# Optimization experiments

Measured on AMD Instinct MI355X. Metric: run time of the kernel, lower is better.

## Reference

```python
import jax, jax.numpy as jnp
import numpy as np
from jax import lax

B = 16384
NWIRES = 4


def _conv(x, w, b):
    # NCHW conv, stride 1, SAME padding (pad 1 for k=3)
    y = lax.conv_general_dilated(x, w, (1, 1), ((1, 1), (1, 1)),
                                 dimension_numbers=("NCHW", "OIHW", "NCHW"))
    return y + b[None, :, None, None]


def _pool2(x):
    b, c, h, w = x.shape
    return x.reshape(b, c, h // 2, 2, w // 2, 2).max(axis=(3, 5))


def _apply_1q(state, U, wire):
    # state: (B,2,2,2,2) complex; U: (B,2,2) complex
    s = jnp.moveaxis(state, wire + 1, -1)
    s = jnp.einsum("bij,b...j->b...i", U, s)
    return jnp.moveaxis(s, -1, wire + 1)


def _apply_cnot(state, c, t):
    s0 = jnp.take(state, 0, axis=c + 1)
    s1 = jnp.take(state, 1, axis=c + 1)
    ta = t + 1 if t < c else t  # target axis index after removing control axis
    s1 = jnp.flip(s1, axis=ta)
    return jnp.stack([s0, s1], axis=c + 1)


def _ry(th):
    c = jnp.cos(th / 2)
    s = jnp.sin(th / 2)
    U = jnp.stack([jnp.stack([c, -s], -1), jnp.stack([s, c], -1)], -2)
    return U.astype(jnp.complex64)


def _rz(th):
    e = jnp.exp(-0.5j * th.astype(jnp.complex64))
    z = jnp.zeros_like(e)
    return jnp.stack([jnp.stack([e, z], -1), jnp.stack([z, jnp.conj(e)], -1)], -2)


def _rx(th):
    c = jnp.cos(th / 2).astype(jnp.complex64)
    s = jnp.sin(th / 2).astype(jnp.complex64)
    return jnp.stack([jnp.stack([c, -1j * s], -1), jnp.stack([-1j * s, c], -1)], -2)


def _circuit(params):
    # params: (B, 16) -> PauliZ expvals (B, 4)
    b = params.shape[0]
    state = jnp.zeros((b, 16), jnp.complex64).at[:, 0].set(1.0).reshape(b, 2, 2, 2, 2)
    for i in range(NWIRES):
        state = _apply_1q(state, _ry(params[:, 4 * i + 0]), i)
        state = _apply_1q(state, _rz(params[:, 4 * i + 1]), i)
        state = _apply_1q(state, _rx(params[:, 4 * i + 2]), i)
        state = _apply_cnot(state, i, (i + 1) % NWIRES)
    probs = state.real ** 2 + state.imag ** 2  # (B,2,2,2,2)
    zs = []
    for i in range(NWIRES):
        p = probs.sum(axis=tuple(a for a in range(1, 5) if a != i + 1))  # (B,2)
        zs.append(p[:, 0] - p[:, 1])
    return jnp.stack(zs, axis=-1)


def setup_inputs() -> dict:
    key = jax.random.key(0)
    ks = jax.random.split(key, 12)
    d = {}
    d["x"] = jax.random.normal(ks[0], (B, 1, 28, 28), jnp.float32)
    d["conv1_w"] = jax.random.normal(ks[1], (4, 1, 3, 3), jnp.float32) * 0.3
    d["conv1_b"] = jax.random.normal(ks[2], (4,), jnp.float32) * 0.1
    d["conv2_w"] = jax.random.normal(ks[3], (4, 4, 3, 3), jnp.float32) * 0.15
    d["conv2_b"] = jax.random.normal(ks[4], (4,), jnp.float32) * 0.1
    d["pl_w"] = jax.random.normal(ks[5], (16, 196), jnp.float32) * 0.07
    d["pl_b"] = jax.random.normal(ks[6], (16,), jnp.float32) * 0.05
    d["ro_w"] = jax.random.normal(ks[7], (4, 4), jnp.float32) * 0.5
    d["ro_b"] = jax.random.normal(ks[8], (4,), jnp.float32) * 0.1
    d["bn_w"] = jnp.ones((4,), jnp.float32)
    d["bn_b"] = jnp.zeros((4,), jnp.float32)
    return d


def reference(x, conv1_w, conv1_b, conv2_w, conv2_b, pl_w, pl_b, ro_w, ro_b, bn_w, bn_b):
    h = _pool2(jax.nn.relu(_conv(x, conv1_w, conv1_b)))   # (B,4,14,14)
    h = _pool2(jax.nn.relu(_conv(h, conv2_w, conv2_b)))   # (B,4,7,7)
    flat = h.reshape(x.shape[0], -1)                      # (B,196)
    params = flat @ pl_w.T + pl_b                         # (B,16)
    z = _circuit(params)                                  # (B,4)
    out = z @ ro_w.T + ro_b                               # (B,4)
    mean = out.mean(0)
    var = out.var(0)  # biased, matches torch BN training normalization
    return (out - mean) / jnp.sqrt(var + 1e-5) * bn_w + bn_b
```

## Files before the change

### kernel.cpp

```cpp
#include <hip/hip_runtime.h>
#include <math.h>

#define BATCH 16384

typedef float v2f __attribute__((ext_vector_type(2)));

__device__ __forceinline__ v2f pk_fma(v2f a, v2f b, v2f c) {
  return __builtin_elementwise_fma(a, b, c);
}
__device__ __forceinline__ v2f pk_max(v2f a, v2f b) {
  return __builtin_elementwise_max(a, b);
}

__device__ __forceinline__ unsigned bf2(float lo, float hi) {
  unsigned a = __float_as_uint(lo);
  unsigned b = __float_as_uint(hi);
  a = (a + 0x7fffu + ((a >> 16) & 1u)) >> 16;
  b = (b + 0x7fffu + ((b >> 16) & 1u)) & 0xffff0000u;
  return a | b;
}

__global__ __launch_bounds__(256) void qnat_fused(
    const float* __restrict__ x,
    const float* __restrict__ w1,
    const float* __restrict__ b1,
    const float* __restrict__ w2,
    const float* __restrict__ b2,
    const float* __restrict__ plw,
    const float* __restrict__ plb,
    const float* __restrict__ rw,
    const float* __restrict__ rb,
    float* __restrict__ pre,
    float* __restrict__ stats)
{
  __shared__ __align__(16) float h1p[4][4 * 288 + 16];
  __shared__ __align__(16) float h2[4][4][200];
  __shared__ __align__(16) uint4 plw_tb[25 * 16];
  __shared__ float s_red[4][8];

  const int tid = threadIdx.x;
  const int w = tid >> 6;
  const int lane = tid & 63;
  const int base = (blockIdx.x * 4 + w) * 4;

  #pragma unroll
  for (int j = 0; j < 2; j++) {
    int s = tid + 256 * j;
    if (s < 400) {
      int tp = s >> 4;
      int k = s & 15;
      const float4* pr = (const float4*)(plw + k * 196);
      float4 a = pr[2 * tp];
      float4 b = (tp < 24) ? pr[2 * tp + 1] : make_float4(0.f, 0.f, 0.f, 0.f);
      plw_tb[s] = make_uint4(bf2(a.x, a.y), bf2(a.z, a.w),
                             bf2(b.x, b.y), bf2(b.z, b.w));
    }
  }

  {
    float4 z4 = make_float4(0.f, 0.f, 0.f, 0.f);
    float4* hz = (float4*)&h1p[w][0];
    #pragma unroll
    for (int t = 0; t < 5; t++) {
      int p = t * 64 + lane;
      if (p < 292) hz[p] = z4;
    }
    if (lane < 16) h2[w][lane >> 2][196 + (lane & 3)] = 0.0f;
  }
  __syncthreads();

  const int i = lane >> 2;
  const int q = lane & 3;
  const bool c1act = lane < 56;

  float4 pfa[4], pfb[4];
  float pe0[4], pe1[4];
  #pragma unroll
  for (int r = 0; r < 4; r++) {
    pfa[r] = make_float4(0,0,0,0); pfb[r] = make_float4(0,0,0,0);
    pe0[r] = 0.0f; pe1[r] = 0.0f;
  }

  if (c1act) {
    const float* xb = x + (size_t)base * 784;
    #pragma unroll
    for (int r = 0; r < 4; r++) {
      int row = 2 * i - 1 + r;
      if (0 <= row && row < 28) {
        const float* rp = xb + row * 28;
        pfa[r] = *(const float4*)(rp + 8 * q);
        if (q > 0) pe0[r] = rp[8 * q - 1];
        if (q < 3) {
          pfb[r] = *(const float4*)(rp + 8 * q + 4);
          pe1[r] = rp[8 * q + 8];
        }
      }
    }
  }

  for (int it = 0; it < 4; ++it) {
    if (c1act) {
      float win[4][10];
      #pragma unroll
      for (int r = 0; r < 4; r++) {
        win[r][0] = pe0[r];
        win[r][1] = pfa[r].x; win[r][2] = pfa[r].y;
        win[r][3] = pfa[r].z; win[r][4] = pfa[r].w;
        win[r][5] = pfb[r].x; win[r][6] = pfb[r].y;
        win[r][7] = pfb[r].z; win[r][8] = pfb[r].w;
        win[r][9] = pe1[r];
      }
      if (it != 3) {
        const float* xn = x + (size_t)(base + it + 1) * 784;
        #pragma unroll
        for (int r = 0; r < 4; r++) {
          int row = 2 * i - 1 + r;
          pfa[r] = make_float4(0,0,0,0);
          pfb[r] = make_float4(0,0,0,0);
          pe0[r] = 0.0f; pe1[r] = 0.0f;
          if (0 <= row && row < 28) {
            const float* rp = xn + row * 28;
            pfa[r] = *(const float4*)(rp + 8 * q);
            if (q > 0) pe0[r] = rp[8 * q - 1];
            if (q < 3) {
              pfb[r] = *(const float4*)(rp + 8 * q + 4);
              pe1[r] = rp[8 * q + 8];
            }
          }
        }
      }
      v2f P[4][9];
      #pragma unroll
      for (int r = 0; r < 4; r++)
        #pragma unroll
        for (int k = 0; k < 9; k++) P[r][k] = (v2f){win[r][k], win[r][k + 1]};

      float* hb = &h1p[w][18 * (i + 1) + 1 + 4 * q];
      #pragma unroll
      for (int c = 0; c < 4; c++) {
        const float* wc = w1 + c * 9;
        const v2f bias2 = (v2f){b1[c], b1[c]};
        v2f a0[4], a1[4];
        #pragma unroll
        for (int jj = 0; jj < 4; jj++) { a0[jj] = bias2; a1[jj] = bias2; }
        #pragma unroll
        for (int dy = 0; dy < 3; dy++)
          #pragma unroll
          for (int dx = 0; dx < 3; dx++) {
            const float wv = wc[dy * 3 + dx];
            const v2f wvv = (v2f){wv, wv};
            #pragma unroll
            for (int jj = 0; jj < 4; jj++) {
              a0[jj] = pk_fma(P[dy][2 * jj + dx],     wvv, a0[jj]);
              a1[jj] = pk_fma(P[dy + 1][2 * jj + dx], wvv, a1[jj]);
            }
          }
        float m[4];
        #pragma unroll
        for (int jj = 0; jj < 4; jj++) {
          v2f mm = pk_max(a0[jj], a1[jj]);
          m[jj] = fmaxf(fmaxf(mm.x, mm.y), 0.0f);
        }
        float* p = hb + 288 * c;
        if (q < 3) {
          p[0] = m[0];
          *(float2*)(p + 1) = make_float2(m[1], m[2]);
          p[3] = m[3];
        } else {
          p[0] = m[0];
          p[1] = m[1];
        }
      }
    }

    {
      const int jq = lane & 7;
      const int i2 = lane >> 3;
      if (i2 < 7 && jq < 7) {
        v2f acc[4][2];
        #pragma unroll
        for (int co = 0; co < 4; co++) {
          const v2f bb = (v2f){b2[co], b2[co]};
          acc[co][0] = bb; acc[co][1] = bb;
        }
        #pragma unroll
        for (int ci = 0; ci < 4; ci++) {
          const float* rp = &h1p[w][288 * ci + 36 * i2 + 2 * jq];
          v2f Q[4][3];
          #pragma unroll
          for (int r = 0; r < 4; r++) {
            v2f a = *(const v2f*)(rp + 18 * r);
            v2f b = *(const v2f*)(rp + 18 * r + 2);
            Q[r][0] = a;
            Q[r][1] = (v2f){a.y, b.x};
            Q[r][2] = b;
          }
          #pragma unroll
          for (int co = 0; co < 4; co++) {
            const float* wp = w2 + (co * 4 + ci) * 9;
            #pragma unroll
            for (int dy = 0; dy < 3; dy++)
              #pragma unroll
              for (int dx = 0; dx < 3; dx++) {
                const float wv = wp[dy * 3 + dx];
                const v2f wvv = (v2f){wv, wv};
                acc[co][0] = pk_fma(Q[dy][dx],     wvv, acc[co][0]);
                acc[co][1] = pk_fma(Q[dy + 1][dx], wvv, acc[co][1]);
              }
          }
        }
        #pragma unroll
        for (int co = 0; co < 4; co++) {
          v2f mm = pk_max(acc[co][0], acc[co][1]);
          h2[w][it][49 * co + 7 * i2 + jq] = fmaxf(fmaxf(mm.x, mm.y), 0.0f);
        }
      }
    }
  }

  const int s2 = lane >> 4;
  const int k = lane & 15;

  float cv, sv;
  {
    const float4* hv4 = (const float4*)&h2[w][s2][0];
    const uint4*  wb4 = &plw_tb[k];
    v2f sacc = (v2f){0.0f, 0.0f};
    #pragma unroll
    for (int t = 0; t < 25; t++) {
      float4 h0 = hv4[2 * t];
      float4 h1 = hv4[2 * t + 1];
      uint4 wb = wb4[16 * t];
      v2f w01 = (v2f){__uint_as_float(wb.x << 16), __uint_as_float(wb.x & 0xffff0000u)};
      v2f w23 = (v2f){__uint_as_float(wb.y << 16), __uint_as_float(wb.y & 0xffff0000u)};
      v2f w45 = (v2f){__uint_as_float(wb.z << 16), __uint_as_float(wb.z & 0xffff0000u)};
      v2f w67 = (v2f){__uint_as_float(wb.w << 16), __uint_as_float(wb.w & 0xffff0000u)};
      sacc = pk_fma((v2f){h0.x, h0.y}, w01, sacc);
      sacc = pk_fma((v2f){h0.z, h0.w}, w23, sacc);
      sacc = pk_fma((v2f){h1.x, h1.y}, w45, sacc);
      sacc = pk_fma((v2f){h1.z, h1.w}, w67, sacc);
    }
    float pv = sacc.x + sacc.y + plb[k];
    __sincosf(pv * 0.5f, &sv, &cv);
  }

  {
    const int l = k;
    const int gb = lane & 48;
    float re = (l == 0) ? 1.0f : 0.0f;
    float im = 0.0f;
    #pragma unroll
    for (int qi = 0; qi < 4; qi++) {
      const int beta = 3 - qi;
      const int m = 1 << beta;
      const int b = (l >> beta) & 1;
      float c = __shfl(cv, gb + 4 * qi, 64), s = __shfl(sv, gb + 4 * qi, 64);
      float pr_ = __shfl_xor(re, m, 64), pi_ = __shfl_xor(im, m, 64);
      float sg = b ? s : -s;
      re = fmaf(c, re, sg * pr_);
      im = fmaf(c, im, sg * pi_);
      c = __shfl(cv, gb + 4 * qi + 1, 64); s = __shfl(sv, gb + 4 * qi + 1, 64);
      float sz = b ? s : -s;
      float nr = c * re - sz * im;
      float ni = c * im + sz * re;
      re = nr; im = ni;
      c = __shfl(cv, gb + 4 * qi + 2, 64); s = __shfl(sv, gb + 4 * qi + 2, 64);
      pr_ = __shfl_xor(re, m, 64); pi_ = __shfl_xor(im, m, 64);
      nr = fmaf(c, re, s * pi_);
      ni = fmaf(c, im, -s * pr_);
      re = nr; im = ni;
      const int tm = 1 << (3 - ((qi + 1) & 3));
      float fr = __shfl_xor(re, tm, 64), fi = __shfl_xor(im, tm, 64);
      if (b) { re = fr; im = fi; }
    }
    float pr2 = re * re + im * im;
    float z0 = ((l >> 3) & 1) ? -pr2 : pr2;
    float z1 = ((l >> 2) & 1) ? -pr2 : pr2;
    float z2 = ((l >> 1) & 1) ? -pr2 : pr2;
    float z3 = (l & 1) ? -pr2 : pr2;
    #pragma unroll
    for (int off = 8; off >= 1; off >>= 1) {
      z0 += __shfl_xor(z0, off, 64);
      z1 += __shfl_xor(z1, off, 64);
      z2 += __shfl_xor(z2, off, 64);
      z3 += __shfl_xor(z3, off, 64);
    }
    float as0 = 0.f, as1 = 0.f, as2 = 0.f, as3 = 0.f;
    float aq0 = 0.f, aq1 = 0.f, aq2 = 0.f, aq3 = 0.f;
    if (l == 0) {
      float o0 = fmaf(rw[0],  z0, fmaf(rw[1],  z1, fmaf(rw[2],  z2, fmaf(rw[3],  z3, rb[0]))));
      float o1 = fmaf(rw[4],  z0, fmaf(rw[5],  z1, fmaf(rw[6],  z2, fmaf(rw[7],  z3, rb[1]))));
      float o2 = fmaf(rw[8],  z0, fmaf(rw[9],  z1, fmaf(rw[10], z2, fmaf(rw[11], z3, rb[2]))));
      float o3 = fmaf(rw[12], z0, fmaf(rw[13], z1, fmaf(rw[14], z2, fmaf(rw[15], z3, rb[3]))));
      *(float4*)(pre + (size_t)(base + s2) * 4) = make_float4(o0, o1, o2, o3);
      as0 = o0; aq0 = o0 * o0;
      as1 = o1; aq1 = o1 * o1;
      as2 = o2; aq2 = o2 * o2;
      as3 = o3; aq3 = o3 * o3;
    }
    #pragma unroll
    for (int off = 32; off >= 16; off >>= 1) {
      as0 += __shfl_down(as0, off, 64); aq0 += __shfl_down(aq0, off, 64);
      as1 += __shfl_down(as1, off, 64); aq1 += __shfl_down(aq1, off, 64);
      as2 += __shfl_down(as2, off, 64); aq2 += __shfl_down(aq2, off, 64);
      as3 += __shfl_down(as3, off, 64); aq3 += __shfl_down(aq3, off, 64);
    }
    if (lane == 0) {
      s_red[w][0] = as0; s_red[w][4] = aq0;
      s_red[w][1] = as1; s_red[w][5] = aq1;
      s_red[w][2] = as2; s_red[w][6] = aq2;
      s_red[w][3] = as3; s_red[w][7] = aq3;
    }
  }
  __syncthreads();
  if (tid < 8) {
    float v = s_red[0][tid] + s_red[1][tid] + s_red[2][tid] + s_red[3][tid];
    atomicAdd(&stats[tid], v);
  }
}

__global__ __launch_bounds__(256) void qnat_bn(
    float* __restrict__ pre,
    const float* __restrict__ stats,
    const float* __restrict__ bnw,
    const float* __restrict__ bnb)
{
  int idx = blockIdx.x * 256 + threadIdx.x;
  int c = idx & 3;
  float mean = stats[c] * (1.0f / BATCH);
  float ex2 = stats[4 + c] * (1.0f / BATCH);
  float var = ex2 - mean * mean;
  float inv = rsqrtf(var + 1e-5f);
  pre[idx] = (pre[idx] - mean) * inv * bnw[c] + bnb[c];
}

extern "C" void kernel_launch(void* const* d_in, const int* in_sizes, int n_in,
                              void* d_out, int out_size, void* d_ws, size_t ws_size,
                              hipStream_t stream) {
  const float* x   = (const float*)d_in[0];
  const float* w1  = (const float*)d_in[1];
  const float* b1  = (const float*)d_in[2];
  const float* w2  = (const float*)d_in[3];
  const float* b2  = (const float*)d_in[4];
  const float* plw = (const float*)d_in[5];
  const float* plb = (const float*)d_in[6];
  const float* rw  = (const float*)d_in[7];
  const float* rb  = (const float*)d_in[8];
  const float* bnw = (const float*)d_in[9];
  const float* bnb = (const float*)d_in[10];

  float* out   = (float*)d_out;
  float* stats = (float*)d_ws;

  hipMemsetAsync(stats, 0, 8 * sizeof(float), stream);
  qnat_fused<<<BATCH / 16, 256, 0, stream>>>(x, w1, b1, w2, b2, plw, plb, rw, rb, out, stats);
  qnat_bn<<<(BATCH * 4) / 256, 256, 0, stream>>>(out, stats, bnw, bnb);
}
```

Before: 134.9 us.

## Store intermediate activations in bf16 LDS and halve samples per wave for occupancy

Intermediate conv activations in shared memory are now stored as packed bf16 with hardware conversion instead of fp32, cutting LDS footprint and traffic. Each wave now handles two samples instead of four, and the grid doubles. The linear layer splits its dot product across two half-waves joined by a shuffle. The register prefetch pipeline for the next sample's input is dropped, and launch bounds request 8 blocks per CU. Together these aim to raise occupancy and hide latency through more resident waves, at the cost of bf16 precision on activations and losing the explicit load prefetch.

Result: slower. 224.1 us (+66.1%).

```diff
diff --git a/kernel.cpp b/kernel.cpp
--- a/kernel.cpp
+++ b/kernel.cpp
@@ -4,6 +4,7 @@
 #define BATCH 16384
 
 typedef float v2f __attribute__((ext_vector_type(2)));
+typedef unsigned short u16;
 
 __device__ __forceinline__ v2f pk_fma(v2f a, v2f b, v2f c) {
   return __builtin_elementwise_fma(a, b, c);
@@ -20,7 +21,15 @@
   return a | b;
 }
 
-__global__ __launch_bounds__(256) void qnat_fused(
+__device__ __forceinline__ unsigned cvtpk(float lo, float hi) {
+  unsigned r;
+  asm("v_cvt_pk_bf16_f32 %0, %1, %2" : "=v"(r) : "v"(lo), "v"(hi));
+  return r;
+}
+__device__ __forceinline__ float blo(unsigned u) { return __uint_as_float(u << 16); }
+__device__ __forceinline__ float bhi(unsigned u) { return __uint_as_float(u & 0xffff0000u); }
+
+__global__ __launch_bounds__(256, 8) void qnat_fused(
     const float* __restrict__ x,
     const float* __restrict__ w1,
     const float* __restrict__ b1,
@@ -33,39 +42,46 @@
     float* __restrict__ pre,
     float* __restrict__ stats)
 {
-  __shared__ __align__(16) float h1p[4][4 * 288 + 16];
-  __shared__ __align__(16) float h2[4][4][200];
-  __shared__ __align__(16) uint4 plw_tb[25 * 16];
+  __shared__ __align__(16) u16 h1s[4][4 * 288];
+  __shared__ __align__(16) u16 h2s[4][2][208];
+  __shared__ __align__(16) uint4 plw_tb[26 * 16];
   __shared__ float s_red[4][8];
 
   const int tid = threadIdx.x;
   const int w = tid >> 6;
   const int lane = tid & 63;
-  const int base = (blockIdx.x * 4 + w) * 4;
+  const int base = (blockIdx.x * 4 + w) * 2;
 
   #pragma unroll
   for (int j = 0; j < 2; j++) {
     int s = tid + 256 * j;
-    if (s < 400) {
+    if (s < 416) {
       int tp = s >> 4;
-      int k = s & 15;
-      const float4* pr = (const float4*)(plw + k * 196);
-      float4 a = pr[2 * tp];
-      float4 b = (tp < 24) ? pr[2 * tp + 1] : make_float4(0.f, 0.f, 0.f, 0.f);
-      plw_tb[s] = make_uint4(bf2(a.x, a.y), bf2(a.z, a.w),
-                             bf2(b.x, b.y), bf2(b.z, b.w));
+      int k2 = s & 15;
+      uint4 v = make_uint4(0u, 0u, 0u, 0u);
+      if (tp < 25) {
+        const float4* pr = (const float4*)(plw + k2 * 196);
+        float4 a = pr[2 * tp];
+        float4 b = (tp < 24) ? pr[2 * tp + 1] : make_float4(0.f, 0.f, 0.f, 0.f);
+        v = make_uint4(bf2(a.x, a.y), bf2(a.z, a.w),
+                       bf2(b.x, b.y), bf2(b.z, b.w));
+      }
+      plw_tb[s] = v;
     }
   }
 
   {
-    float4 z4 = make_float4(0.f, 0.f, 0.f, 0.f);
-    float4* hz = (float4*)&h1p[w][0];
+    uint4 z4 = make_uint4(0u, 0u, 0u, 0u);
+    uint4* hz = (uint4*)&h1s[w][0];
     #pragma unroll
-    for (int t = 0; t < 5; t++) {
+    for (int t = 0; t < 3; t++) {
       int p = t * 64 + lane;
-      if (p < 292) hz[p] = z4;
-    }
-    if (lane < 16) h2[w][lane >> 2][196 + (lane & 3)] = 0.0f;
+      if (p < 144) hz[p] = z4;
+    }
+    if (lane < 4) {
+      uint4* hp4 = (uint4*)&h2s[w][lane >> 1][0];
+      hp4[24 + (lane & 1)] = z4;
+    }
   }
   __syncthreads();
 
@@ -73,69 +89,38 @@
   const int q = lane & 3;
   const bool c1act = lane < 56;
 
-  float4 pfa[4], pfb[4];
-  float pe0[4], pe1[4];
-  #pragma unroll
-  for (int r = 0; r < 4; r++) {
-    pfa[r] = make_float4(0,0,0,0); pfb[r] = make_float4(0,0,0,0);
-    pe0[r] = 0.0f; pe1[r] = 0.0f;
-  }
-
-  if (c1act) {
-    const float* xb = x + (size_t)base * 784;
-    #pragma unroll
-    for (int r = 0; r < 4; r++) {
-      int row = 2 * i - 1 + r;
-      if (0 <= row && row < 28) {
-        const float* rp = xb + row * 28;
-        pfa[r] = *(const float4*)(rp + 8 * q);
-        if (q > 0) pe0[r] = rp[8 * q - 1];
-        if (q < 3) {
-          pfb[r] = *(const float4*)(rp + 8 * q + 4);
-          pe1[r] = rp[8 * q + 8];
-        }
-      }
-    }
-  }
-
-  for (int it = 0; it < 4; ++it) {
+  for (int it = 0; it < 2; ++it) {
     if (c1act) {
       float win[4][10];
+      const float* xb = x + (size_t)(base + it) * 784;
       #pragma unroll
       for (int r = 0; r < 4; r++) {
-        win[r][0] = pe0[r];
-        win[r][1] = pfa[r].x; win[r][2] = pfa[r].y;
-        win[r][3] = pfa[r].z; win[r][4] = pfa[r].w;
-        win[r][5] = pfb[r].x; win[r][6] = pfb[r].y;
-        win[r][7] = pfb[r].z; win[r][8] = pfb[r].w;
-        win[r][9] = pe1[r];
-      }
-      if (it != 3) {
-        const float* xn = x + (size_t)(base + it + 1) * 784;
-        #pragma unroll
-        for (int r = 0; r < 4; r++) {
-          int row = 2 * i - 1 + r;
-          pfa[r] = make_float4(0,0,0,0);
-          pfb[r] = make_float4(0,0,0,0);
-          pe0[r] = 0.0f; pe1[r] = 0.0f;
-          if (0 <= row && row < 28) {
-            const float* rp = xn + row * 28;
-            pfa[r] = *(const float4*)(rp + 8 * q);
-            if (q > 0) pe0[r] = rp[8 * q - 1];
-            if (q < 3) {
-              pfb[r] = *(const float4*)(rp + 8 * q + 4);
-              pe1[r] = rp[8 * q + 8];
-            }
+        int row = 2 * i - 1 + r;
+        if (0 <= row && row < 28) {
+          const float* rp = xb + row * 28;
+          win[r][0] = (q > 0) ? rp[8 * q - 1] : 0.0f;
+          float4 a = *(const float4*)(rp + 8 * q);
+          win[r][1] = a.x; win[r][2] = a.y; win[r][3] = a.z; win[r][4] = a.w;
+          if (q < 3) {
+            float4 b = *(const float4*)(rp + 8 * q + 4);
+            win[r][5] = b.x; win[r][6] = b.y; win[r][7] = b.z; win[r][8] = b.w;
+            win[r][9] = rp[8 * q + 8];
+          } else {
+            win[r][5] = 0.f; win[r][6] = 0.f; win[r][7] = 0.f;
+            win[r][8] = 0.f; win[r][9] = 0.f;
           }
+        } else {
+          #pragma unroll
+          for (int kk = 0; kk < 10; kk++) win[r][kk] = 0.0f;
         }
       }
       v2f P[4][9];
       #pragma unroll
       for (int r = 0; r < 4; r++)
         #pragma unroll
-        for (int k = 0; k < 9; k++) P[r][k] = (v2f){win[r][k], win[r][k + 1]};
-
-      float* hb = &h1p[w][18 * (i + 1) + 1 + 4 * q];
+        for (int kk = 0; kk < 9; kk++) P[r][kk] = (v2f){win[r][kk], win[r][kk + 1]};
+
+      u16* hb = &h1s[w][18 * (i + 1) + 1 + 4 * q];
       #pragma unroll
       for (int c = 0; c < 4; c++) {
         const float* wc = w1 + c * 9;
@@ -161,14 +146,17 @@
           v2f mm = pk_max(a0[jj], a1[jj]);
           m[jj] = fmaxf(fmaxf(mm.x, mm.y), 0.0f);
         }
-        float* p = hb + 288 * c;
+        u16* p = hb + 288 * c;
         if (q < 3) {
-          p[0] = m[0];
-          *(float2*)(p + 1) = make_float2(m[1], m[2]);
-          p[3] = m[3];
+          unsigned u03 = cvtpk(m[0], m[3]);
+          unsigned u12 = cvtpk(m[1], m[2]);
+          p[0] = (u16)u03;
+          *(unsigned*)(p + 1) = u12;
+          p[3] = (u16)(u03 >> 16);
         } else {
-          p[0] = m[0];
-          p[1] = m[1];
+          unsigned u01 = cvtpk(m[0], m[1]);
+          p[0] = (u16)u01;
+          p[1] = (u16)(u01 >> 16);
         }
       }
     }
@@ -185,15 +173,16 @@
         }
         #pragma unroll
         for (int ci = 0; ci < 4; ci++) {
-          const float* rp = &h1p[w][288 * ci + 36 * i2 + 2 * jq];
+          const u16* rp = &h1s[w][288 * ci + 36 * i2 + 2 * jq];
           v2f Q[4][3];
           #pragma unroll
           for (int r = 0; r < 4; r++) {
-            v2f a = *(const v2f*)(rp + 18 * r);
-            v2f b = *(const v2f*)(rp + 18 * r + 2);
-            Q[r][0] = a;
-            Q[r][1] = (v2f){a.y, b.x};
-            Q[r][2] = b;
+            unsigned u0 = *(const unsigned*)(rp + 18 * r);
+            unsigned u1 = *(const unsigned*)(rp + 18 * r + 2);
+            float f0 = blo(u0), f1 = bhi(u0), f2 = blo(u1), f3 = bhi(u1);
+            Q[r][0] = (v2f){f0, f1};
+            Q[r][1] = (v2f){f1, f2};
+            Q[r][2] = (v2f){f2, f3};
           }
           #pragma unroll
           for (int co = 0; co < 4; co++) {
@@ -209,38 +198,45 @@
               }
           }
         }
+        float mo[4];
         #pragma unroll
         for (int co = 0; co < 4; co++) {
           v2f mm = pk_max(acc[co][0], acc[co][1]);
-          h2[w][it][49 * co + 7 * i2 + jq] = fmaxf(fmaxf(mm.x, mm.y), 0.0f);
-        }
+          mo[co] = fmaxf(fmaxf(mm.x, mm.y), 0.0f);
+        }
+        unsigned u01 = cvtpk(mo[0], mo[1]);
+        unsigned u23 = cvtpk(mo[2], mo[3]);
+        u16* hp = &h2s[w][it][7 * i2 + jq];
+        hp[0]   = (u16)u01;
+        hp[49]  = (u16)(u01 >> 16);
+        hp[98]  = (u16)u23;
+        hp[147] = (u16)(u23 >> 16);
       }
     }
   }
 
-  const int s2 = lane >> 4;
+  const int s2 = lane >> 5;
+  const int half = (lane >> 4) & 1;
   const int k = lane & 15;
 
   float cv, sv;
   {
-    const float4* hv4 = (const float4*)&h2[w][s2][0];
-    const uint4*  wb4 = &plw_tb[k];
+    const uint4* hb4 = (const uint4*)&h2s[w][s2][0];
+    const uint4* wb4 = &plw_tb[k];
     v2f sacc = (v2f){0.0f, 0.0f};
     #pragma unroll
-    for (int t = 0; t < 25; t++) {
-      float4 h0 = hv4[2 * t];
-      float4 h1 = hv4[2 * t + 1];
+    for (int tt = 0; tt < 13; tt++) {
+      int t = 2 * tt + half;
+      uint4 hb = hb4[t];
       uint4 wb = wb4[16 * t];
-      v2f w01 = (v2f){__uint_as_float(wb.x << 16), __uint_as_float(wb.x & 0xffff0000u)};
-      v2f w23 = (v2f){__uint_as_float(wb.y << 16), __uint_as_float(wb.y & 0xffff0000u)};
-      v2f w45 = (v2f){__uint_as_float(wb.z << 16), __uint_as_float(wb.z & 0xffff0000u)};
-      v2f w67 = (v2f){__uint_as_float(wb.w << 16), __uint_as_float(wb.w & 0xffff0000u)};
-      sacc = pk_fma((v2f){h0.x, h0.y}, w01, sacc);
-      sacc = pk_fma((v2f){h0.z, h0.w}, w23, sacc);
-      sacc = pk_fma((v2f){h1.x, h1.y}, w45, sacc);
-      sacc = pk_fma((v2f){h1.z, h1.w}, w67, sacc);
-    }
-    float pv = sacc.x + sacc.y + plb[k];
+      sacc = pk_fma((v2f){blo(hb.x), bhi(hb.x)}, (v2f){blo(wb.x), bhi(wb.x)}, sacc);
+      sacc = pk_fma((v2f){blo(hb.y), bhi(hb.y)}, (v2f){blo(wb.y), bhi(wb.y)}, sacc);
+      sacc = pk_fma((v2f){blo(hb.z), bhi(hb.z)}, (v2f){blo(wb.z), bhi(wb.z)}, sacc);
+      sacc = pk_fma((v2f){blo(hb.w), bhi(hb.w)}, (v2f){blo(wb.w), bhi(wb.w)}, sacc);
+    }
+    float pv = sacc.x + sacc.y;
+    pv += __shfl_xor(pv, 16, 64);
+    pv += plb[k];
     __sincosf(pv * 0.5f, &sv, &cv);
   }
 
@@ -287,7 +283,7 @@
     }
     float as0 = 0.f, as1 = 0.f, as2 = 0.f, as3 = 0.f;
     float aq0 = 0.f, aq1 = 0.f, aq2 = 0.f, aq3 = 0.f;
-    if (l == 0) {
+    if (l == 0 && (lane & 16) == 0) {
       float o0 = fmaf(rw[0],  z0, fmaf(rw[1],  z1, fmaf(rw[2],  z2, fmaf(rw[3],  z3, rb[0]))));
       float o1 = fmaf(rw[4],  z0, fmaf(rw[5],  z1, fmaf(rw[6],  z2, fmaf(rw[7],  z3, rb[1]))));
       float o2 = fmaf(rw[8],  z0, fmaf(rw[9],  z1, fmaf(rw[10], z2, fmaf(rw[11], z3, rb[2]))));
@@ -298,13 +294,10 @@
       as2 = o2; aq2 = o2 * o2;
       as3 = o3; aq3 = o3 * o3;
     }
-    #pragma unroll
-    for (int off = 32; off >= 16; off >>= 1) {
-      as0 += __shfl_down(as0, off, 64); aq0 += __shfl_down(aq0, off, 64);
-      as1 += __shfl_down(as1, off, 64); aq1 += __shfl_down(aq1, off, 64);
-      as2 += __shfl_down(as2, off, 64); aq2 += __shfl_down(aq2, off, 64);
-      as3 += __shfl_down(as3, off, 64); aq3 += __shfl_down(aq3, off, 64);
-    }
+    as0 += __shfl_down(as0, 32, 64); aq0 += __shfl_down(aq0, 32, 64);
+    as1 += __shfl_down(as1, 32, 64); aq1 += __shfl_down(aq1, 32, 64);
+    as2 += __shfl_down(as2, 32, 64); aq2 += __shfl_down(aq2, 32, 64);
+    as3 += __shfl_down(as3, 32, 64); aq3 += __shfl_down(aq3, 32, 64);
     if (lane == 0) {
       s_red[w][0] = as0; s_red[w][4] = aq0;
       s_red[w][1] = as1; s_red[w][5] = aq1;
@@ -353,6 +346,6 @@
   float* stats = (float*)d_ws;
 
   hipMemsetAsync(stats, 0, 8 * sizeof(float), stream);
-  qnat_fused<<<BATCH / 16, 256, 0, stream>>>(x, w1, b1, w2, b2, plw, plb, rw, rb, out, stats);
+  qnat_fused<<<BATCH / 8, 256, 0, stream>>>(x, w1, b1, w2, b2, plw, plb, rw, rb, out, stats);
   qnat_bn<<<(BATCH * 4) / 256, 256, 0, stream>>>(out, stats, bnw, bnb);
 }
```
